# Kernel optimization log

Measured on AMD Instinct MI355X. Metric: run time of the kernel, lower is better.

The kernel has to match this reference:

```python
import jax, jax.numpy as jnp
import numpy as np


def _shift(x):
    # x: [B, C, H, W]; split channels into 5 groups: 4 of size C//5, remainder unshifted
    B, C, H, W = x.shape
    g = C // 5
    x0 = x[:, 0*g:1*g]
    x1 = x[:, 1*g:2*g]
    x2 = x[:, 2*g:3*g]
    x3 = x[:, 3*g:4*g]
    x4 = x[:, 4*g:]
    # shift down (roll +1 along H), zero first row
    r0 = jnp.roll(x0, 1, axis=2).at[:, :, 0, :].set(0.0)
    # shift left (roll -1 along W), zero last col
    r1 = jnp.roll(x1, -1, axis=3).at[:, :, :, W - 1].set(0.0)
    # shift up (roll -1 along H), zero last row
    r2 = jnp.roll(x2, -1, axis=2).at[:, :, H - 1, :].set(0.0)
    # shift right (roll +1 along W), zero first col
    r3 = jnp.roll(x3, 1, axis=3).at[:, :, :, 0].set(0.0)
    return jnp.concatenate([r0, r1, r2, r3, x4], axis=1)


def setup_inputs() -> dict:
    key = jax.random.key(0)
    x = jax.random.normal(key, (64, 256, 56, 56), dtype=jnp.float32)
    return {"x": x}


def reference(x):
    return _shift(x)
```

## Files before the change

### kernel.cpp

```cpp
#include <hip/hip_runtime.h>

constexpr int B  = 64;
constexpr int C  = 256;
constexpr int H  = 56;
constexpr int W  = 56;
constexpr int G  = 51;
constexpr int W4 = W / 4;
constexpr int N4 = B * C * H * W4;

__global__ __launch_bounds__(256) void shift_kernel(const float* __restrict__ in,
                                                    float* __restrict__ out) {
    const int stride = gridDim.x * blockDim.x;
    for (int i = blockIdx.x * blockDim.x + threadIdx.x; i < N4; i += stride) {
        const int w4 = i % W4;
        const int t  = i / W4;
        const int h  = t % H;
        const int c  = (t / H) % C;

        const int row_base = t * W;
        const int idx      = row_base + 4 * w4;

        float4 r;
        if (c < G) {
            if (h == 0) {
                r = make_float4(0.f, 0.f, 0.f, 0.f);
            } else {
                r = *reinterpret_cast<const float4*>(in + idx - W);
            }
        } else if (c < 2 * G) {
            const float4 v = *reinterpret_cast<const float4*>(in + idx);
            const float  s = (w4 == W4 - 1) ? 0.f : in[idx + 4];
            r = make_float4(v.y, v.z, v.w, s);
        } else if (c < 3 * G) {
            if (h == H - 1) {
                r = make_float4(0.f, 0.f, 0.f, 0.f);
            } else {
                r = *reinterpret_cast<const float4*>(in + idx + W);
            }
        } else if (c < 4 * G) {
            const float4 v = *reinterpret_cast<const float4*>(in + idx);
            const float  s = (w4 == 0) ? 0.f : in[idx - 1];
            r = make_float4(s, v.x, v.y, v.z);
        } else {
            r = *reinterpret_cast<const float4*>(in + idx);
        }
        *reinterpret_cast<float4*>(out + idx) = r;
    }
}

extern "C" void kernel_launch(void* const* d_in, const int* in_sizes, int n_in,
                              void* d_out, int out_size, void* d_ws, size_t ws_size,
                              hipStream_t stream) {
    const float* in  = (const float*)d_in[0];
    float*       out = (float*)d_out;
    dim3 grid(2048), block(256);
    hipLaunchKernelGGL(shift_kernel, grid, block, 0, stream, in, out);
}
```

Baseline: 78.57 us.

## Batch four float4 loads per thread, use wave shuffles for W shifts, nontemporal stores

Replaces the grid-stride loop with a fixed grid where each thread issues four independent float4 loads up front, raising memory-level parallelism. The horizontal-shift groups get their neighbour element through cross-lane shuffles instead of a second scalar global load, with edge lanes falling back to a global read. Group selection becomes branch-light arithmetic, and outputs use nontemporal stores to avoid polluting cache. The added complexity risks register pressure, and shuffle correctness depends on adjacent lanes holding adjacent w4 within a row.

```diff
diff --git a/kernel.cpp b/kernel.cpp
--- a/kernel.cpp
+++ b/kernel.cpp
@@ -7,44 +7,69 @@
 constexpr int G  = 51;
 constexpr int W4 = W / 4;
 constexpr int N4 = B * C * H * W4;
+constexpr int ITEMS = 4;
+constexpr int BLOCK = 256;
+constexpr int TILE  = BLOCK * ITEMS;
+constexpr int NBLK  = N4 / TILE;
 
-__global__ __launch_bounds__(256) void shift_kernel(const float* __restrict__ in,
-                                                    float* __restrict__ out) {
-    const int stride = gridDim.x * blockDim.x;
-    for (int i = blockIdx.x * blockDim.x + threadIdx.x; i < N4; i += stride) {
+typedef float f4 __attribute__((ext_vector_type(4)));
+
+__global__ __launch_bounds__(BLOCK) void shift_kernel(const float* __restrict__ in,
+                                                      float* __restrict__ out) {
+    const int tid  = threadIdx.x;
+    const int lane = tid & 63;
+    const int i0   = blockIdx.x * TILE + tid;
+
+    int idx[ITEMS];
+    int gg[ITEMS];
+    int w4a[ITEMS];
+    f4  v[ITEMS];
+
+    #pragma unroll
+    for (int k = 0; k < ITEMS; ++k) {
+        const int i  = i0 + k * BLOCK;
         const int w4 = i % W4;
         const int t  = i / W4;
-        const int h  = t % H;
-        const int c  = (t / H) % C;
+        const int u  = t / H;
+        const int h  = t - u * H;
+        const int c  = u & (C - 1);
 
-        const int row_base = t * W;
-        const int idx      = row_base + 4 * w4;
+        idx[k] = 4 * i;
+        w4a[k] = w4;
 
-        float4 r;
-        if (c < G) {
-            if (h == 0) {
-                r = make_float4(0.f, 0.f, 0.f, 0.f);
-            } else {
-                r = *reinterpret_cast<const float4*>(in + idx - W);
-            }
-        } else if (c < 2 * G) {
-            const float4 v = *reinterpret_cast<const float4*>(in + idx);
-            const float  s = (w4 == W4 - 1) ? 0.f : in[idx + 4];
-            r = make_float4(v.y, v.z, v.w, s);
-        } else if (c < 3 * G) {
-            if (h == H - 1) {
-                r = make_float4(0.f, 0.f, 0.f, 0.f);
-            } else {
-                r = *reinterpret_cast<const float4*>(in + idx + W);
-            }
-        } else if (c < 4 * G) {
-            const float4 v = *reinterpret_cast<const float4*>(in + idx);
-            const float  s = (w4 == 0) ? 0.f : in[idx - 1];
-            r = make_float4(s, v.x, v.y, v.z);
-        } else {
-            r = *reinterpret_cast<const float4*>(in + idx);
-        }
-        *reinterpret_cast<float4*>(out + idx) = r;
+        const int g = (c >= G) + (c >= 2 * G) + (c >= 3 * G) + (c >= 4 * G);
+        gg[k] = g;
+
+        const bool invalid = (g == 0 && h == 0) || (g == 2 && h == H - 1);
+        const int  off     = (g == 0) ? -W : (g == 2) ? W : 0;
+        const int  src     = invalid ? idx[k] : idx[k] + off;
+
+        f4 x = *reinterpret_cast<const f4*>(in + src);
+        if (invalid) x = (f4){0.f, 0.f, 0.f, 0.f};
+        v[k] = x;
+    }
+
+    #pragma unroll
+    for (int k = 0; k < ITEMS; ++k) {
+        const int w4 = w4a[k];
+        const int g  = gg[k];
+        const f4  x  = v[k];
+
+        const float nxtx = __shfl_down(x.x, 1, 64);
+        const float prvw = __shfl_up(x.w, 1, 64);
+
+        float nxt = (w4 == W4 - 1) ? 0.f : nxtx;
+        float prv = (w4 == 0)      ? 0.f : prvw;
+
+        if (g == 1 && lane == 63 && w4 != W4 - 1) nxt = in[idx[k] + 4];
+        if (g == 3 && lane == 0  && w4 != 0)      prv = in[idx[k] - 1];
+
+        f4 r;
+        if (g == 1)      r = (f4){x.y, x.z, x.w, nxt};
+        else if (g == 3) r = (f4){prv, x.x, x.y, x.z};
+        else             r = x;
+
+        __builtin_nontemporal_store(r, reinterpret_cast<f4*>(out + idx[k]));
     }
 }
 
@@ -53,6 +78,5 @@
                               hipStream_t stream) {
     const float* in  = (const float*)d_in[0];
     float*       out = (float*)d_out;
-    dim3 grid(2048), block(256);
-    hipLaunchKernelGGL(shift_kernel, grid, block, 0, stream, in, out);
+    hipLaunchKernelGGL(shift_kernel, dim3(NBLK), dim3(BLOCK), 0, stream, in, out);
 }
```

Result: faster. 64.20 us (-18.3%).
